# Optimization experiments

Measured on AMD Instinct MI355X. Metric: run time of the kernel, lower is better.

The kernel has to match this reference:

```python
import jax, jax.numpy as jnp
import numpy as np

NEG = jnp.finfo(jnp.float32).min


def setup_inputs() -> dict:
    key = jax.random.key(0)
    k1, k2, k3 = jax.random.split(key, 3)
    B, H, S, D = 1, 12, 4096, 64
    query = jax.random.normal(k1, (B, H, S, D), dtype=jnp.float32)
    key_t = jax.random.normal(k2, (B, H, S, D), dtype=jnp.float32)
    value = jax.random.normal(k3, (B, H, S, D), dtype=jnp.float32)
    attention_mask = jnp.ones((B, S), dtype=jnp.int32)  # 2D mask -> causal branch
    return {
        "query": query,
        "key": key_t,
        "value": value,
        "attention_mask": attention_mask,
        "sliding_window": 128,
    }


def reference(query, key, value, attention_mask, sliding_window):
    # query/key/value: [B, H, S, D]
    B, H, S, D = query.shape
    scaling = 1.0 / jnp.sqrt(jnp.float32(D))
    # QK^T scaled: [B, H, S, S]
    attn_weights = jnp.einsum("bhqd,bhkd->bhqk", query, key) * scaling
    i = jnp.arange(S)[:, None]
    j = jnp.arange(S)[None, :]
    # 2D attention_mask branch: causal triu mask (values of mask not used)
    causal_mask = jnp.where(j > i, NEG, 0.0).astype(attn_weights.dtype)
    attn_weights = attn_weights + causal_mask
    # sliding window: row i allows columns [max(0, i - sw + 1), i]
    sw_allowed = (j >= i - sliding_window + 1) & (j <= i)
    sw_mask = jnp.where(sw_allowed, 0.0, NEG).astype(jnp.float32)
    attn_weights = attn_weights + sw_mask[None, None, :, :]
    # softmax in float32, cast back to query dtype
    attn_weights = jax.nn.softmax(attn_weights.astype(jnp.float32), axis=-1).astype(query.dtype)
    # probs @ V, then transpose heads: [B, S, H, D]
    attn_output = jnp.einsum("bhqk,bhkd->bhqd", attn_weights, value)
    attn_output = jnp.transpose(attn_output, (0, 2, 1, 3))
    return attn_output, attn_weights
```

## Files before the change

kernel.cpp:

```cpp
#include <hip/hip_runtime.h>
#include <math.h>

#define NH 12
#define SEQ 4096
#define DIM 64
#define SW 128
#define RPB 16
#define TPB 256
#define KSTRIDE 65
#define MAXK (RPB + SW - 1)
#define BAND_BLOCKS (NH * (SEQ / RPB))
#define FILL_BLOCKS 8192
#define NCHUNK ((size_t)NH * SEQ * (SEQ / 4))

__global__ __launch_bounds__(TPB)
void attn_fused_kernel(const float* __restrict__ Q, const float* __restrict__ K,
                       const float* __restrict__ V, float* __restrict__ Wout,
                       float* __restrict__ Oout) {
    __shared__ float KV[MAXK * KSTRIDE];
    __shared__ float Qs[RPB * DIM];
    __shared__ float Ps[RPB * SW];

    if (blockIdx.x >= BAND_BLOCKS) {
        const size_t tid0   = (size_t)(blockIdx.x - BAND_BLOCKS) * TPB + threadIdx.x;
        const size_t stride = (size_t)FILL_BLOCKS * TPB;
        const float4 z = make_float4(0.f, 0.f, 0.f, 0.f);
        for (size_t idx = tid0; idx < NCHUNK; idx += stride) {
            const int ci = (int)(idx & 1023);
            const int i  = (int)((idx >> 10) & 4095);
            const int w0 = max(0, i - (SW - 1));
            const int cstart = w0 >> 2;
            const int cend   = i >> 2;
            if (ci < cstart || ci > cend) {
                *(float4*)((float*)Wout + idx * 4) = z;
            }
        }
        return;
    }

    const int h    = blockIdx.x / (SEQ / RPB);
    const int tile = blockIdx.x % (SEQ / RPB);
    const int r0   = tile * RPB;
    const int kLo  = max(0, r0 - (SW - 1));
    const int kHi  = r0 + RPB - 1;
    const int nK   = kHi - kLo + 1;

    const float* Qh = Q + (size_t)h * SEQ * DIM;
    const float* Kh = K + (size_t)h * SEQ * DIM;
    const float* Vh = V + (size_t)h * SEQ * DIM;

    const int tid = threadIdx.x;

    for (int idx = tid; idx < nK * (DIM / 4); idx += TPB) {
        const int row = idx >> 4;
        const int c4  = (idx & 15) * 4;
        const float4 v = *(const float4*)(Kh + (size_t)(kLo + row) * DIM + c4);
        float* dst = &KV[row * KSTRIDE + c4];
        dst[0] = v.x; dst[1] = v.y; dst[2] = v.z; dst[3] = v.w;
    }
    for (int idx = tid; idx < RPB * (DIM / 4); idx += TPB) {
        const int row = idx >> 4;
        const int c4  = (idx & 15) * 4;
        *(float4*)&Qs[row * DIM + c4] =
            *(const float4*)(Qh + (size_t)(r0 + row) * DIM + c4);
    }
    __syncthreads();

    const int wave = tid >> 6;
    const int lane = tid & 63;
    const float scale = 0.125f;

    for (int t = 0; t < 4; ++t) {
        const int r  = wave * 4 + t;
        const int i  = r0 + r;
        const int w0 = max(0, i - (SW - 1));

        float s0 = -INFINITY, s1 = -INFINITY;
        {
            const int col = w0 + lane;
            if (col <= i) {
                const float* kr = &KV[(col - kLo) * KSTRIDE];
                const float* qr = &Qs[r * DIM];
                float acc = 0.f;
                #pragma unroll
                for (int d = 0; d < DIM; ++d) acc += qr[d] * kr[d];
                s0 = acc * scale;
            }
        }
        {
            const int col = w0 + 64 + lane;
            if (col <= i) {
                const float* kr = &KV[(col - kLo) * KSTRIDE];
                const float* qr = &Qs[r * DIM];
                float acc = 0.f;
                #pragma unroll
                for (int d = 0; d < DIM; ++d) acc += qr[d] * kr[d];
                s1 = acc * scale;
            }
        }
        float m = fmaxf(s0, s1);
        #pragma unroll
        for (int o = 32; o > 0; o >>= 1) m = fmaxf(m, __shfl_xor(m, o, 64));
        const float e0 = __expf(s0 - m);
        const float e1 = __expf(s1 - m);
        float sum = e0 + e1;
        #pragma unroll
        for (int o = 32; o > 0; o >>= 1) sum += __shfl_xor(sum, o, 64);
        const float inv = 1.0f / sum;
        Ps[r * SW + lane]      = e0 * inv;
        Ps[r * SW + 64 + lane] = e1 * inv;
    }
    __syncthreads();

    for (int idx = tid; idx < nK * (DIM / 4); idx += TPB) {
        const int row = idx >> 4;
        const int c4  = (idx & 15) * 4;
        *(float4*)&KV[row * DIM + c4] =
            *(const float4*)(Vh + (size_t)(kLo + row) * DIM + c4);
    }
    __syncthreads();

    {
        const int rbase = wave * 4;
        const int i0 = r0 + rbase;
        const int u0 = max(0, i0 - (SW - 1));
        const int u1 = i0 + 3;

        float acc0 = 0.f, acc1 = 0.f, acc2 = 0.f, acc3 = 0.f;
        for (int j = u0; j <= u1; ++j) {
            const float v = KV[(j - kLo) * DIM + lane];
            {   const int i = i0 + 0, w0 = max(0, i - (SW - 1)), rel = j - w0;
                if (rel >= 0 && j <= i) acc0 += Ps[(rbase + 0) * SW + rel] * v; }
            {   const int i = i0 + 1, w0 = max(0, i - (SW - 1)), rel = j - w0;
                if (rel >= 0 && j <= i) acc1 += Ps[(rbase + 1) * SW + rel] * v; }
            {   const int i = i0 + 2, w0 = max(0, i - (SW - 1)), rel = j - w0;
                if (rel >= 0 && j <= i) acc2 += Ps[(rbase + 2) * SW + rel] * v; }
            {   const int i = i0 + 3, w0 = max(0, i - (SW - 1)), rel = j - w0;
                if (rel >= 0 && j <= i) acc3 += Ps[(rbase + 3) * SW + rel] * v; }
        }
        Oout[((size_t)(i0 + 0) * NH + h) * DIM + lane] = acc0;
        Oout[((size_t)(i0 + 1) * NH + h) * DIM + lane] = acc1;
        Oout[((size_t)(i0 + 2) * NH + h) * DIM + lane] = acc2;
        Oout[((size_t)(i0 + 3) * NH + h) * DIM + lane] = acc3;

        #pragma unroll
        for (int t = 0; t < 4; ++t) {
            const int r  = rbase + t;
            const int i  = r0 + r;
            const int w0 = max(0, i - (SW - 1));
            const int cstart = w0 >> 2;
            const int cend   = i >> 2;
            const int c = cstart + lane;
            if (c <= cend) {
                const int col0 = c * 4;
                float vv[4];
                #pragma unroll
                for (int k = 0; k < 4; ++k) {
                    const int col = col0 + k;
                    const int rel = min(max(col - w0, 0), SW - 1);
                    const float p = Ps[r * SW + rel];
                    vv[k] = (col >= w0 && col <= i) ? p : 0.f;
                }
                float* wrow = Wout + ((size_t)(h * SEQ + i)) * SEQ;
                *(float4*)(wrow + col0) = make_float4(vv[0], vv[1], vv[2], vv[3]);
            }
        }
    }
}

extern "C" void kernel_launch(void* const* d_in, const int* in_sizes, int n_in,
                              void* d_out, int out_size, void* d_ws, size_t ws_size,
                              hipStream_t stream) {
    const float* Q = (const float*)d_in[0];
    const float* K = (const float*)d_in[1];
    const float* V = (const float*)d_in[2];

    float* Oout = (float*)d_out;
    float* Wout = (float*)d_out + (size_t)SEQ * NH * DIM;

    dim3 grid(BAND_BLOCKS + FILL_BLOCKS);
    attn_fused_kernel<<<grid, TPB, 0, stream>>>(Q, K, V, Wout, Oout);
}
```

Measured before the change: 1.019 ms.

## Interleave band and fill blocks, swizzle K in LDS, vectorise PV

Result: faster. 862.2 us (-15.4%).

```diff
diff --git a/kernel.cpp b/kernel.cpp
--- a/kernel.cpp
+++ b/kernel.cpp
@@ -7,62 +7,67 @@
 #define SW 128
 #define RPB 16
 #define TPB 256
-#define KSTRIDE 65
 #define MAXK (RPB + SW - 1)
+#define PSTRIDE 144
 #define BAND_BLOCKS (NH * (SEQ / RPB))
-#define FILL_BLOCKS 8192
+#define FILL_BLOCKS 8448
+#define PERIOD 15
 #define NCHUNK ((size_t)NH * SEQ * (SEQ / 4))
 
-__global__ __launch_bounds__(TPB)
-void attn_fused_kernel(const float* __restrict__ Q, const float* __restrict__ K,
-                       const float* __restrict__ V, float* __restrict__ Wout,
-                       float* __restrict__ Oout) {
-    __shared__ float KV[MAXK * KSTRIDE];
-    __shared__ float Qs[RPB * DIM];
-    __shared__ float Ps[RPB * SW];
+typedef float v4f __attribute__((ext_vector_type(4)));
 
-    if (blockIdx.x >= BAND_BLOCKS) {
-        const size_t tid0   = (size_t)(blockIdx.x - BAND_BLOCKS) * TPB + threadIdx.x;
+__global__ __launch_bounds__(TPB, 3)
+void attn_fused2(const float* __restrict__ Q, const float* __restrict__ K,
+                 const float* __restrict__ V, float* __restrict__ Wout,
+                 float* __restrict__ Oout) {
+    __shared__ v4f KV4[MAXK * 16];
+    __shared__ __align__(16) float Qs[RPB * DIM];
+    __shared__ v4f Ps4[RPB * (PSTRIDE / 4)];
+    float* Ps = (float*)Ps4;
+
+    const int grp = blockIdx.x / PERIOD;
+    const int rem = blockIdx.x % PERIOD;
+
+    if (rem >= 4) {
+        const size_t fid   = (size_t)grp * 11 + (rem - 4);
+        const size_t tid0  = fid * TPB + threadIdx.x;
         const size_t stride = (size_t)FILL_BLOCKS * TPB;
         const float4 z = make_float4(0.f, 0.f, 0.f, 0.f);
         for (size_t idx = tid0; idx < NCHUNK; idx += stride) {
             const int ci = (int)(idx & 1023);
             const int i  = (int)((idx >> 10) & 4095);
             const int w0 = max(0, i - (SW - 1));
-            const int cstart = w0 >> 2;
-            const int cend   = i >> 2;
-            if (ci < cstart || ci > cend) {
+            if (ci < (w0 >> 2) || ci > (i >> 2)) {
                 *(float4*)((float*)Wout + idx * 4) = z;
             }
         }
         return;
     }
 
-    const int h    = blockIdx.x / (SEQ / RPB);
-    const int tile = blockIdx.x % (SEQ / RPB);
+    const int bid  = grp * 4 + rem;
+    const int h    = bid / (SEQ / RPB);
+    const int tile = bid % (SEQ / RPB);
     const int r0   = tile * RPB;
     const int kLo  = max(0, r0 - (SW - 1));
-    const int kHi  = r0 + RPB - 1;
-    const int nK   = kHi - kLo + 1;
+    const int nK   = r0 + RPB - kLo;
 
     const float* Qh = Q + (size_t)h * SEQ * DIM;
     const float* Kh = K + (size_t)h * SEQ * DIM;
     const float* Vh = V + (size_t)h * SEQ * DIM;
-
     const int tid = threadIdx.x;
 
-    for (int idx = tid; idx < nK * (DIM / 4); idx += TPB) {
-        const int row = idx >> 4;
-        const int c4  = (idx & 15) * 4;
-        const float4 v = *(const float4*)(Kh + (size_t)(kLo + row) * DIM + c4);
-        float* dst = &KV[row * KSTRIDE + c4];
-        dst[0] = v.x; dst[1] = v.y; dst[2] = v.z; dst[3] = v.w;
+    for (int idx = tid; idx < MAXK * 16; idx += TPB) {
+        const int c = idx >> 4, b = idx & 15;
+        const int src = min(c, nK - 1);
+        KV4[c * 16 + (b ^ (c & 15))] =
+            *(const v4f*)(Kh + (size_t)(kLo + src) * DIM + b * 4);
     }
-    for (int idx = tid; idx < RPB * (DIM / 4); idx += TPB) {
-        const int row = idx >> 4;
-        const int c4  = (idx & 15) * 4;
-        *(float4*)&Qs[row * DIM + c4] =
-            *(const float4*)(Qh + (size_t)(r0 + row) * DIM + c4);
+    {
+        const int r = tid >> 4, b = tid & 15;
+        *(v4f*)&Qs[r * 64 + b * 4] = *(const v4f*)(Qh + (size_t)(r0 + r) * DIM + b * 4);
+    }
+    for (int idx = tid; idx < RPB * (PSTRIDE / 4); idx += TPB) {
+        Ps4[idx] = (v4f){0.f, 0.f, 0.f, 0.f};
     }
     __syncthreads();
 
@@ -74,30 +79,32 @@
         const int r  = wave * 4 + t;
         const int i  = r0 + r;
         const int w0 = max(0, i - (SW - 1));
+        const int c0 = w0 - kLo;
 
-        float s0 = -INFINITY, s1 = -INFINITY;
-        {
-            const int col = w0 + lane;
-            if (col <= i) {
-                const float* kr = &KV[(col - kLo) * KSTRIDE];
-                const float* qr = &Qs[r * DIM];
-                float acc = 0.f;
-                #pragma unroll
-                for (int d = 0; d < DIM; ++d) acc += qr[d] * kr[d];
-                s0 = acc * scale;
-            }
+        v4f q[16];
+        #pragma unroll
+        for (int b = 0; b < 16; ++b) q[b] = *(const v4f*)&Qs[r * 64 + b * 4];
+
+        const int cA = c0 + lane;
+        float accA = 0.f;
+        #pragma unroll
+        for (int b = 0; b < 16; ++b) {
+            const v4f kv = KV4[cA * 16 + (b ^ (cA & 15))];
+            accA += q[b].x * kv.x + q[b].y * kv.y + q[b].z * kv.z + q[b].w * kv.w;
         }
-        {
-            const int col = w0 + 64 + lane;
-            if (col <= i) {
-                const float* kr = &KV[(col - kLo) * KSTRIDE];
-                const float* qr = &Qs[r * DIM];
-                float acc = 0.f;
-                #pragma unroll
-                for (int d = 0; d < DIM; ++d) acc += qr[d] * kr[d];
-                s1 = acc * scale;
-            }
+        const int colA = w0 + lane;
+        const float s0 = (colA <= i) ? accA * scale : -INFINITY;
+
+        const int cB = cA + 64;
+        float accB = 0.f;
+        #pragma unroll
+        for (int b = 0; b < 16; ++b) {
+            const v4f kv = KV4[cB * 16 + (b ^ (cB & 15))];
+            accB += q[b].x * kv.x + q[b].y * kv.y + q[b].z * kv.z + q[b].w * kv.w;
         }
+        const int colB = colA + 64;
+        const float s1 = (colB <= i) ? accB * scale : -INFINITY;
+
         float m = fmaxf(s0, s1);
         #pragma unroll
         for (int o = 32; o > 0; o >>= 1) m = fmaxf(m, __shfl_xor(m, o, 64));
@@ -107,64 +114,57 @@
         #pragma unroll
         for (int o = 32; o > 0; o >>= 1) sum += __shfl_xor(sum, o, 64);
         const float inv = 1.0f / sum;
-        Ps[r * SW + lane]      = e0 * inv;
-        Ps[r * SW + 64 + lane] = e1 * inv;
+        const float p0 = e0 * inv, p1 = e1 * inv;
+
+        Ps[r * PSTRIDE + c0 + lane]      = p0;
+        Ps[r * PSTRIDE + c0 + 64 + lane] = p1;
+
+        float* wrow = Wout + ((size_t)h * SEQ + i) * SEQ;
+        if (colA <= i) wrow[colA] = p0;
+        if (colB <= i) wrow[colB] = p1;
+        if (lane < 4) {
+            const int cl = (w0 & ~3) + lane;
+            if (cl < w0) wrow[cl] = 0.f;
+            const int ch = i + 1 + lane;
+            if (ch <= (i | 3)) wrow[ch] = 0.f;
+        }
     }
     __syncthreads();
 
-    for (int idx = tid; idx < nK * (DIM / 4); idx += TPB) {
-        const int row = idx >> 4;
-        const int c4  = (idx & 15) * 4;
-        *(float4*)&KV[row * DIM + c4] =
-            *(const float4*)(Vh + (size_t)(kLo + row) * DIM + c4);
+    for (int idx = tid; idx < MAXK * 16; idx += TPB) {
+        const int c = idx >> 4, b = idx & 15;
+        const int src = min(c, nK - 1);
+        KV4[c * 16 + b] = *(const v4f*)(Vh + (size_t)(kLo + src) * DIM + b * 4);
     }
     __syncthreads();
 
     {
         const int rbase = wave * 4;
-        const int i0 = r0 + rbase;
-        const int u0 = max(0, i0 - (SW - 1));
-        const int u1 = i0 + 3;
+        const int i0  = r0 + rbase;
+        const int u0k = max(0, i0 - (SW - 1)) - kLo;
+        const int u1k = i0 + 3 - kLo;
+        const int nch = (u1k - u0k + 4) >> 2;
+        const int q4  = lane >> 4, l16 = lane & 15;
 
-        float acc0 = 0.f, acc1 = 0.f, acc2 = 0.f, acc3 = 0.f;
-        for (int j = u0; j <= u1; ++j) {
-            const float v = KV[(j - kLo) * DIM + lane];
-            {   const int i = i0 + 0, w0 = max(0, i - (SW - 1)), rel = j - w0;
-                if (rel >= 0 && j <= i) acc0 += Ps[(rbase + 0) * SW + rel] * v; }
-            {   const int i = i0 + 1, w0 = max(0, i - (SW - 1)), rel = j - w0;
-                if (rel >= 0 && j <= i) acc1 += Ps[(rbase + 1) * SW + rel] * v; }
-            {   const int i = i0 + 2, w0 = max(0, i - (SW - 1)), rel = j - w0;
-                if (rel >= 0 && j <= i) acc2 += Ps[(rbase + 2) * SW + rel] * v; }
-            {   const int i = i0 + 3, w0 = max(0, i - (SW - 1)), rel = j - w0;
-                if (rel >= 0 && j <= i) acc3 += Ps[(rbase + 3) * SW + rel] * v; }
+        v4f a0 = {0.f,0.f,0.f,0.f}, a1 = a0, a2 = a0, a3 = a0;
+        for (int k = 0; k < nch; ++k) {
+            const int cc = u0k + k * 4 + q4;
+            const v4f vv = KV4[cc * 16 + l16];
+            a0 += Ps[(rbase + 0) * PSTRIDE + cc] * vv;
+            a1 += Ps[(rbase + 1) * PSTRIDE + cc] * vv;
+            a2 += Ps[(rbase + 2) * PSTRIDE + cc] * vv;
+            a3 += Ps[(rbase + 3) * PSTRIDE + cc] * vv;
         }
-        Oout[((size_t)(i0 + 0) * NH + h) * DIM + lane] = acc0;
-        Oout[((size_t)(i0 + 1) * NH + h) * DIM + lane] = acc1;
-        Oout[((size_t)(i0 + 2) * NH + h) * DIM + lane] = acc2;
-        Oout[((size_t)(i0 + 3) * NH + h) * DIM + lane] = acc3;
-
         #pragma unroll
-        for (int t = 0; t < 4; ++t) {
-            const int r  = rbase + t;
-            const int i  = r0 + r;
-            const int w0 = max(0, i - (SW - 1));
-            const int cstart = w0 >> 2;
-            const int cend   = i >> 2;
-            const int c = cstart + lane;
-            if (c <= cend) {
-                const int col0 = c * 4;
-                float vv[4];
-                #pragma unroll
-                for (int k = 0; k < 4; ++k) {
-                    const int col = col0 + k;
-                    const int rel = min(max(col - w0, 0), SW - 1);
-                    const float p = Ps[r * SW + rel];
-                    vv[k] = (col >= w0 && col <= i) ? p : 0.f;
-                }
-                float* wrow = Wout + ((size_t)(h * SEQ + i)) * SEQ;
-                *(float4*)(wrow + col0) = make_float4(vv[0], vv[1], vv[2], vv[3]);
-            }
+        for (int c = 0; c < 4; ++c) {
+            float v;
+            v = a0[c]; v += __shfl_xor(v, 16, 64); v += __shfl_xor(v, 32, 64); a0[c] = v;
+            v = a1[c]; v += __shfl_xor(v, 16, 64); v += __shfl_xor(v, 32, 64); a1[c] = v;
+            v = a2[c]; v += __shfl_xor(v, 16, 64); v += __shfl_xor(v, 32, 64); a2[c] = v;
+            v = a3[c]; v += __shfl_xor(v, 16, 64); v += __shfl_xor(v, 32, 64); a3[c] = v;
         }
+        const v4f o = (q4 == 0) ? a0 : (q4 == 1) ? a1 : (q4 == 2) ? a2 : a3;
+        *(v4f*)(Oout + ((size_t)(i0 + q4) * NH + h) * DIM + l16 * 4) = o;
     }
 }
 
@@ -179,5 +179,5 @@
     float* Wout = (float*)d_out + (size_t)SEQ * NH * DIM;
 
     dim3 grid(BAND_BLOCKS + FILL_BLOCKS);
-    attn_fused_kernel<<<grid, TPB, 0, stream>>>(Q, K, V, Wout, Oout);
+    attn_fused2<<<grid, TPB, 0, stream>>>(Q, K, V, Wout, Oout);
 }
```
